# Kernel tuning notes

Hardware: AMD Instinct MI355X
Metric: run time of the kernel (lower is better)

The kernel has to match this reference:

```python
import jax, jax.numpy as jnp
import numpy as np

QUALITY = 50.0
TEMP = 0.3  # soft-round temperature

_LUM = np.array([[16,11,10,16,24,40,51,61],[12,12,14,19,26,58,60,55],[14,13,16,24,40,57,69,56],[14,17,22,29,51,87,80,62],[18,22,37,56,68,109,103,77],[24,35,55,64,81,104,113,92],[49,64,78,87,103,121,120,101],[72,92,95,98,112,100,103,99]], dtype=np.float32)
_CHR = np.array([[17,18,24,47,99,99,99,99],[18,21,26,66,99,99,99,99],[24,26,56,99,99,99,99,99],[47,66,99,99,99,99,99,99],[99,99,99,99,99,99,99,99],[99,99,99,99,99,99,99,99],[99,99,99,99,99,99,99,99],[99,99,99,99,99,99,99,99]], dtype=np.float32)

def _scaled_qtable(base, qf):
    qf = max(1.0, min(100.0, qf))
    s = 5000.0 / qf if qf < 50 else 200.0 - 2.0 * qf
    return np.maximum(np.floor((base * s + 50.0) / 100.0), 1.0)

# Per-channel quantization tables: Y uses luminance, Cb/Cr use chrominance. (3,8,8)
QTAB = jnp.asarray(np.stack([_scaled_qtable(_LUM, QUALITY), _scaled_qtable(_CHR, QUALITY), _scaled_qtable(_CHR, QUALITY)]).astype(np.float32))

# The original 64x1x8x8 conv kernel factors as outer product D[u,x]*D[v,y].
_u = np.arange(8)[:, None]
_x = np.arange(8)[None, :]
_c = np.where(_u == 0, 1.0 / np.sqrt(2.0), 1.0)
DCT = jnp.asarray((0.5 * _c * np.cos((2 * _x + 1) * _u * np.pi / 16.0)).astype(np.float32))

M_FWD = jnp.array([[0.299, 0.587, 0.114], [-0.168736, -0.331264, 0.5], [0.5, -0.418688, -0.081312]], dtype=jnp.float32)
M_INV = jnp.array([[1.0, 0.0, 1.402], [1.0, -0.344136, -0.714136], [1.0, 1.772, 0.0]], dtype=jnp.float32)
OFF = jnp.array([0.0, 0.5, 0.5], dtype=jnp.float32)


def setup_inputs() -> dict:
    key = jax.random.key(0)
    x = jax.random.uniform(key, (32, 3, 512, 512), dtype=jnp.float32)
    return {"x": x}


def reference(x):
    B, C, H, W = x.shape  # H, W divisible by 8 (no pad branch)
    # RGB -> YCbCr, centered
    ycbcr = jnp.einsum('ij,bjhw->bihw', M_FWD, x) + OFF[None, :, None, None] - 0.5
    # split into 8x8 blocks: (B, 3, H/8, 8, W/8, 8)
    blocks = ycbcr.reshape(B, C, H // 8, 8, W // 8, 8)
    # block DCT: coef[u,v] = sum_{x,y} D[u,x] D[v,y] block[x,y]
    coef = jnp.einsum('ux,vy,bchxgy->bchugv', DCT, DCT, blocks)
    q = QTAB[None, :, None, :, None, :]  # broadcast per-channel table
    d = coef / q
    # smooth rounding: x + 0.5*tanh(50*T*(x - round(x)))
    sr = d + 0.5 * jnp.tanh(50.0 * TEMP * (d - jnp.round(d)))
    deq = sr * q
    # block IDCT (transpose of DCT): block[x,y] = sum_{u,v} D[u,x] D[v,y] coef[u,v]
    rec = jnp.einsum('ux,vy,bchugv->bchxgy', DCT, DCT, deq)
    ycbcr_rec = rec.reshape(B, C, H, W) + 0.5
    rgb = jnp.einsum('ij,bjhw->bihw', M_INV, ycbcr_rec - OFF[None, :, None, None])
    return jnp.clip(rgb, 0.0, 1.0)
```

## Files before the change

### kernel.cpp

```cpp
#include <hip/hip_runtime.h>
#include <math.h>

#define A0c 0.35355339059327373f
#define C1c 0.4903926402016152f
#define C2c 0.46193976625564337f
#define C3c 0.41573480615127262f
#define C5c 0.27778511650980114f
#define C6c 0.19134171618254492f
#define C7c 0.09754516100806417f

#define IMG_W 512
#define IMG_HW (512 * 512)

typedef float f8v __attribute__((ext_vector_type(8)));

__device__ const float QLUM[64] = {
    16,11,10,16,24,40,51,61,  12,12,14,19,26,58,60,55,
    14,13,16,24,40,57,69,56,  14,17,22,29,51,87,80,62,
    18,22,37,56,68,109,103,77, 24,35,55,64,81,104,113,92,
    49,64,78,87,103,121,120,101, 72,92,95,98,112,100,103,99};
__device__ const float QCHR[64] = {
    17,18,24,47,99,99,99,99,  18,21,26,66,99,99,99,99,
    24,26,56,99,99,99,99,99,  47,66,99,99,99,99,99,99,
    99,99,99,99,99,99,99,99,  99,99,99,99,99,99,99,99,
    99,99,99,99,99,99,99,99,  99,99,99,99,99,99,99,99};

__device__ __forceinline__ void fdct8(float v[8]) {
    float s0 = v[0] + v[7], s1 = v[1] + v[6], s2 = v[2] + v[5], s3 = v[3] + v[4];
    float d0 = v[0] - v[7], d1 = v[1] - v[6], d2 = v[2] - v[5], d3 = v[3] - v[4];
    float e0 = s0 + s3, e1 = s1 + s2, f0 = s0 - s3, f1 = s1 - s2;
    v[0] = A0c * (e0 + e1);
    v[4] = A0c * (e0 - e1);
    v[2] = C2c * f0 + C6c * f1;
    v[6] = C6c * f0 - C2c * f1;
    v[1] = C1c * d0 + C3c * d1 + C5c * d2 + C7c * d3;
    v[3] = C3c * d0 - C7c * d1 - C1c * d2 - C5c * d3;
    v[5] = C5c * d0 - C1c * d1 + C7c * d2 + C3c * d3;
    v[7] = C7c * d0 - C5c * d1 + C3c * d2 - C1c * d3;
}

__device__ __forceinline__ void idct8(float v[8]) {
    float g0 = v[0], g1 = v[1], g2 = v[2], g3 = v[3];
    float g4 = v[4], g5 = v[5], g6 = v[6], g7 = v[7];
    float ep = A0c * (g0 + g4), em = A0c * (g0 - g4);
    float t26a = C2c * g2 + C6c * g6;
    float t26b = C6c * g2 - C2c * g6;
    float e0 = ep + t26a, e1 = em + t26b, e2 = em - t26b, e3 = ep - t26a;
    float o0 = C1c * g1 + C3c * g3 + C5c * g5 + C7c * g7;
    float o1 = C3c * g1 - C7c * g3 - C1c * g5 - C5c * g7;
    float o2 = C5c * g1 - C1c * g3 + C7c * g5 + C3c * g7;
    float o3 = C7c * g1 - C5c * g3 + C3c * g5 - C1c * g7;
    v[0] = e0 + o0; v[7] = e0 - o0;
    v[1] = e1 + o1; v[6] = e1 - o1;
    v[2] = e2 + o2; v[5] = e2 - o2;
    v[3] = e3 + o3; v[4] = e3 - o3;
}

__device__ __forceinline__ float softq(float x, float q, float rq) {
    float d = x * rq;
    float rn = rintf(d);
    float t = d - rn;
    float e = __expf(-30.0f * fabsf(t));
    float th = (1.0f - e) * __builtin_amdgcn_rcpf(1.0f + e);
    th = copysignf(th, t);
    return (d + 0.5f * th) * q;
}

__device__ __forceinline__ void midchain(float w[8], const float* qrow) {
    fdct8(w);
#pragma unroll
    for (int u = 0; u < 8; ++u) {
        float q = qrow[u];
        w[u] = softq(w[u], q, __builtin_amdgcn_rcpf(q));
    }
    idct8(w);
}

__global__ __launch_bounds__(256) void jpeg_kernel(const float* __restrict__ x,
                                                   float* __restrict__ out) {
    __shared__ float xpose[4][3][576];
    __shared__ float qt[2][64];

    const int tid = threadIdx.x;
    const int wid = tid >> 6;
    const int lane = tid & 63;

    {
        int u = lane & 7, v = lane >> 3;
        qt[0][lane] = QLUM[u * 8 + v];
        qt[1][lane] = QCHR[u * 8 + v];
    }

    const int gw = blockIdx.x * 4 + wid;
    const int bimg = gw >> 9;
    const int rem = gw & 511;
    const int gh = rem >> 3;
    const int tx = rem & 7;

    const int blk = lane & 7;
    const int row = lane >> 3;

    const float* base = x + (size_t)bimg * 3 * IMG_HW +
                        (size_t)(gh * 8 + row) * IMG_W + tx * 64 + blk * 8;
    float* obase = out + (size_t)bimg * 3 * IMG_HW +
                   (size_t)(gh * 8 + row) * IMG_W + tx * 64 + blk * 8;

    const f8v Rv = *(const f8v*)(base);
    const f8v Gv = *(const f8v*)(base + IMG_HW);
    const f8v Bv = *(const f8v*)(base + 2 * IMG_HW);

    float* xp0 = xpose[wid][0];
    float* xp1 = xpose[wid][1];
    float* xp2 = xpose[wid][2];
    const int wi = blk * 9 + row;

    float g0[8], g1[8], g2[8];
#pragma unroll
    for (int k = 0; k < 8; ++k) {
        float R = Rv[k], G = Gv[k], B = Bv[k];
        g0[k] = 0.299f * R + 0.587f * G + 0.114f * B - 0.5f;
        g1[k] = -0.168736f * R - 0.331264f * G + 0.5f * B;
        g2[k] = 0.5f * R - 0.418688f * G - 0.081312f * B;
    }
    fdct8(g0); fdct8(g1); fdct8(g2);

#pragma unroll
    for (int v = 0; v < 8; ++v) xp0[v * 72 + wi] = g0[v];
#pragma unroll
    for (int v = 0; v < 8; ++v) xp1[v * 72 + wi] = g1[v];
#pragma unroll
    for (int v = 0; v < 8; ++v) xp2[v * 72 + wi] = g2[v];

    const int ri = row * 72 + blk * 9;
#pragma unroll
    for (int k = 0; k < 8; ++k) g0[k] = xp0[ri + k];
#pragma unroll
    for (int k = 0; k < 8; ++k) g1[k] = xp1[ri + k];
#pragma unroll
    for (int k = 0; k < 8; ++k) g2[k] = xp2[ri + k];

    midchain(g0, &qt[0][row * 8]);
#pragma unroll
    for (int k = 0; k < 8; ++k) xp0[ri + k] = g0[k];
    midchain(g1, &qt[1][row * 8]);
#pragma unroll
    for (int k = 0; k < 8; ++k) xp1[ri + k] = g1[k];
#pragma unroll
    for (int v = 0; v < 8; ++v) g0[v] = xp0[v * 72 + wi];
    midchain(g2, &qt[1][row * 8]);
#pragma unroll
    for (int k = 0; k < 8; ++k) xp2[ri + k] = g2[k];
#pragma unroll
    for (int v = 0; v < 8; ++v) g1[v] = xp1[v * 72 + wi];
#pragma unroll
    for (int v = 0; v < 8; ++v) g2[v] = xp2[v * 72 + wi];

    idct8(g0); idct8(g1); idct8(g2);

    f8v Ro, Go, Bo;
#pragma unroll
    for (int k = 0; k < 8; ++k) {
        float Y  = g0[k] + 0.5f;
        float Cb = g1[k];
        float Cr = g2[k];
        float R = Y + 1.402f * Cr;
        float G = Y - 0.344136f * Cb - 0.714136f * Cr;
        float B = Y + 1.772f * Cb;
        Ro[k] = fminf(fmaxf(R, 0.0f), 1.0f);
        Go[k] = fminf(fmaxf(G, 0.0f), 1.0f);
        Bo[k] = fminf(fmaxf(B, 0.0f), 1.0f);
    }
    *(f8v*)(obase) = Ro;
    *(f8v*)(obase + IMG_HW) = Go;
    *(f8v*)(obase + 2 * IMG_HW) = Bo;
}

extern "C" void kernel_launch(void* const* d_in, const int* in_sizes, int n_in,
                              void* d_out, int out_size, void* d_ws, size_t ws_size,
                              hipStream_t stream) {
    const float* x = (const float*)d_in[0];
    float* out = (float*)d_out;
    const int B = in_sizes[0] / (3 * IMG_HW);
    const int n_wg = B * 128;
    hipLaunchKernelGGL(jpeg_kernel, dim3(n_wg), dim3(256), 0, stream, x, out);
}
```

Before: 40.51 us.

## Process channels serially through one LDS buffer and simplify soft-rounding

Shrinks the per-wave shared-memory transpose buffer from three channels to one by running the full DCT, quantise and IDCT chain channel by channel. This lowers LDS use per block and may allow more resident blocks. The soft round now uses exp2 directly with the sign folded in, and returns x + q/2*tanh, using precomputed half-q and reciprocal tables. It relies on compiler-only memory fences for ordering within a wave instead of a barrier. The kernel is likely limited by memory bandwidth, so the compute and occupancy savings may not show.

After: 38.78 us. -4.3%, faster.

```diff
diff --git a/kernel.cpp b/kernel.cpp
--- a/kernel.cpp
+++ b/kernel.cpp
@@ -56,40 +56,26 @@
     v[3] = e3 + o3; v[4] = e3 - o3;
 }
 
-__device__ __forceinline__ float softq(float x, float q, float rq) {
+#define K_EXP2 43.2808512266689f
+__device__ __forceinline__ float softq(float x, float qh, float rq) {
     float d = x * rq;
     float rn = rintf(d);
     float t = d - rn;
-    float e = __expf(-30.0f * fabsf(t));
-    float th = (1.0f - e) * __builtin_amdgcn_rcpf(1.0f + e);
-    th = copysignf(th, t);
-    return (d + 0.5f * th) * q;
-}
-
-__device__ __forceinline__ void midchain(float w[8], const float* qrow) {
-    fdct8(w);
-#pragma unroll
-    for (int u = 0; u < 8; ++u) {
-        float q = qrow[u];
-        w[u] = softq(w[u], q, __builtin_amdgcn_rcpf(q));
-    }
-    idct8(w);
-}
+    float e2 = __builtin_amdgcn_exp2f(K_EXP2 * t);
+    float th = (e2 - 1.0f) * __builtin_amdgcn_rcpf(e2 + 1.0f);
+    return x + qh * th;
+}
+
+#define LDS_FENCE() asm volatile("" ::: "memory")
 
 __global__ __launch_bounds__(256) void jpeg_kernel(const float* __restrict__ x,
                                                    float* __restrict__ out) {
-    __shared__ float xpose[4][3][576];
-    __shared__ float qt[2][64];
+    __shared__ float xpose[4][576];
+    __shared__ float qtab[4][64];
 
     const int tid = threadIdx.x;
     const int wid = tid >> 6;
     const int lane = tid & 63;
-
-    {
-        int u = lane & 7, v = lane >> 3;
-        qt[0][lane] = QLUM[u * 8 + v];
-        qt[1][lane] = QCHR[u * 8 + v];
-    }
 
     const int gw = blockIdx.x * 4 + wid;
     const int bimg = gw >> 9;
@@ -100,19 +86,29 @@
     const int blk = lane & 7;
     const int row = lane >> 3;
 
-    const float* base = x + (size_t)bimg * 3 * IMG_HW +
-                        (size_t)(gh * 8 + row) * IMG_W + tx * 64 + blk * 8;
-    float* obase = out + (size_t)bimg * 3 * IMG_HW +
-                   (size_t)(gh * 8 + row) * IMG_W + tx * 64 + blk * 8;
+    const size_t off = (size_t)bimg * 3 * IMG_HW +
+                       (size_t)(gh * 8 + row) * IMG_W + tx * 64 + blk * 8;
+    const float* base = x + off;
 
     const f8v Rv = *(const f8v*)(base);
     const f8v Gv = *(const f8v*)(base + IMG_HW);
     const f8v Bv = *(const f8v*)(base + 2 * IMG_HW);
 
-    float* xp0 = xpose[wid][0];
-    float* xp1 = xpose[wid][1];
-    float* xp2 = xpose[wid][2];
-    const int wi = blk * 9 + row;
+    {
+        int u = lane & 7, v = lane >> 3;
+        float ql = QLUM[u * 8 + v];
+        float qc = QCHR[u * 8 + v];
+        qtab[0][lane] = 0.5f * ql;
+        qtab[1][lane] = __builtin_amdgcn_rcpf(ql);
+        qtab[2][lane] = 0.5f * qc;
+        qtab[3][lane] = __builtin_amdgcn_rcpf(qc);
+    }
+    LDS_FENCE();
+
+    float* xp = xpose[wid];
+    const int wbase = blk * 9 + row;
+    const int rbase = row * 72 + blk * 9;
+    const int qrow = row * 8;
 
     float g0[8], g1[8], g2[8];
 #pragma unroll
@@ -122,40 +118,90 @@
         g1[k] = -0.168736f * R - 0.331264f * G + 0.5f * B;
         g2[k] = 0.5f * R - 0.418688f * G - 0.081312f * B;
     }
-    fdct8(g0); fdct8(g1); fdct8(g2);
-
-#pragma unroll
-    for (int v = 0; v < 8; ++v) xp0[v * 72 + wi] = g0[v];
-#pragma unroll
-    for (int v = 0; v < 8; ++v) xp1[v * 72 + wi] = g1[v];
-#pragma unroll
-    for (int v = 0; v < 8; ++v) xp2[v * 72 + wi] = g2[v];
-
-    const int ri = row * 72 + blk * 9;
-#pragma unroll
-    for (int k = 0; k < 8; ++k) g0[k] = xp0[ri + k];
-#pragma unroll
-    for (int k = 0; k < 8; ++k) g1[k] = xp1[ri + k];
-#pragma unroll
-    for (int k = 0; k < 8; ++k) g2[k] = xp2[ri + k];
-
-    midchain(g0, &qt[0][row * 8]);
-#pragma unroll
-    for (int k = 0; k < 8; ++k) xp0[ri + k] = g0[k];
-    midchain(g1, &qt[1][row * 8]);
-#pragma unroll
-    for (int k = 0; k < 8; ++k) xp1[ri + k] = g1[k];
-#pragma unroll
-    for (int v = 0; v < 8; ++v) g0[v] = xp0[v * 72 + wi];
-    midchain(g2, &qt[1][row * 8]);
-#pragma unroll
-    for (int k = 0; k < 8; ++k) xp2[ri + k] = g2[k];
-#pragma unroll
-    for (int v = 0; v < 8; ++v) g1[v] = xp1[v * 72 + wi];
-#pragma unroll
-    for (int v = 0; v < 8; ++v) g2[v] = xp2[v * 72 + wi];
-
-    idct8(g0); idct8(g1); idct8(g2);
+
+    fdct8(g0);
+#pragma unroll
+    for (int j = 0; j < 8; ++j) xp[j * 72 + wbase] = g0[j];
+    LDS_FENCE();
+#pragma unroll
+    for (int k = 0; k < 8; ++k) g0[k] = xp[rbase + k];
+    LDS_FENCE();
+    fdct8(g0);
+    {
+        float4 qa = *(const float4*)&qtab[0][qrow];
+        float4 qb = *(const float4*)&qtab[0][qrow + 4];
+        float4 ra = *(const float4*)&qtab[1][qrow];
+        float4 rb = *(const float4*)&qtab[1][qrow + 4];
+        g0[0] = softq(g0[0], qa.x, ra.x); g0[1] = softq(g0[1], qa.y, ra.y);
+        g0[2] = softq(g0[2], qa.z, ra.z); g0[3] = softq(g0[3], qa.w, ra.w);
+        g0[4] = softq(g0[4], qb.x, rb.x); g0[5] = softq(g0[5], qb.y, rb.y);
+        g0[6] = softq(g0[6], qb.z, rb.z); g0[7] = softq(g0[7], qb.w, rb.w);
+    }
+    idct8(g0);
+    LDS_FENCE();
+#pragma unroll
+    for (int j = 0; j < 8; ++j) xp[j * 72 + wbase] = g0[j];
+    LDS_FENCE();
+#pragma unroll
+    for (int k = 0; k < 8; ++k) g0[k] = xp[rbase + k];
+    LDS_FENCE();
+    idct8(g0);
+
+    fdct8(g1);
+#pragma unroll
+    for (int j = 0; j < 8; ++j) xp[j * 72 + wbase] = g1[j];
+    LDS_FENCE();
+#pragma unroll
+    for (int k = 0; k < 8; ++k) g1[k] = xp[rbase + k];
+    LDS_FENCE();
+    fdct8(g1);
+    {
+        float4 qa = *(const float4*)&qtab[2][qrow];
+        float4 qb = *(const float4*)&qtab[2][qrow + 4];
+        float4 ra = *(const float4*)&qtab[3][qrow];
+        float4 rb = *(const float4*)&qtab[3][qrow + 4];
+        g1[0] = softq(g1[0], qa.x, ra.x); g1[1] = softq(g1[1], qa.y, ra.y);
+        g1[2] = softq(g1[2], qa.z, ra.z); g1[3] = softq(g1[3], qa.w, ra.w);
+        g1[4] = softq(g1[4], qb.x, rb.x); g1[5] = softq(g1[5], qb.y, rb.y);
+        g1[6] = softq(g1[6], qb.z, rb.z); g1[7] = softq(g1[7], qb.w, rb.w);
+    }
+    idct8(g1);
+    LDS_FENCE();
+#pragma unroll
+    for (int j = 0; j < 8; ++j) xp[j * 72 + wbase] = g1[j];
+    LDS_FENCE();
+#pragma unroll
+    for (int k = 0; k < 8; ++k) g1[k] = xp[rbase + k];
+    LDS_FENCE();
+    idct8(g1);
+
+    fdct8(g2);
+#pragma unroll
+    for (int j = 0; j < 8; ++j) xp[j * 72 + wbase] = g2[j];
+    LDS_FENCE();
+#pragma unroll
+    for (int k = 0; k < 8; ++k) g2[k] = xp[rbase + k];
+    LDS_FENCE();
+    fdct8(g2);
+    {
+        float4 qa = *(const float4*)&qtab[2][qrow];
+        float4 qb = *(const float4*)&qtab[2][qrow + 4];
+        float4 ra = *(const float4*)&qtab[3][qrow];
+        float4 rb = *(const float4*)&qtab[3][qrow + 4];
+        g2[0] = softq(g2[0], qa.x, ra.x); g2[1] = softq(g2[1], qa.y, ra.y);
+        g2[2] = softq(g2[2], qa.z, ra.z); g2[3] = softq(g2[3], qa.w, ra.w);
+        g2[4] = softq(g2[4], qb.x, rb.x); g2[5] = softq(g2[5], qb.y, rb.y);
+        g2[6] = softq(g2[6], qb.z, rb.z); g2[7] = softq(g2[7], qb.w, rb.w);
+    }
+    idct8(g2);
+    LDS_FENCE();
+#pragma unroll
+    for (int j = 0; j < 8; ++j) xp[j * 72 + wbase] = g2[j];
+    LDS_FENCE();
+#pragma unroll
+    for (int k = 0; k < 8; ++k) g2[k] = xp[rbase + k];
+    LDS_FENCE();
+    idct8(g2);
 
     f8v Ro, Go, Bo;
 #pragma unroll
@@ -170,6 +216,7 @@
         Go[k] = fminf(fmaxf(G, 0.0f), 1.0f);
         Bo[k] = fminf(fmaxf(B, 0.0f), 1.0f);
     }
+    float* obase = out + off;
     *(f8v*)(obase) = Ro;
     *(f8v*)(obase + IMG_HW) = Go;
     *(f8v*)(obase + 2 * IMG_HW) = Bo;
```
